# Optimization experiments

Measured on AMD Instinct MI355X. Metric: run time of the kernel, lower is better.

The kernel has to match this reference:

```python
import jax, jax.numpy as jnp
import numpy as np

IN_F = 4096
OUT_F = 4096
RANK = 16
ALPHA = 32
BLOCK = 64  # quantization blocksize along in_features
SCALING = ALPHA / RANK


def setup_inputs() -> dict:
    key = jax.random.key(0)
    k1, k2, k3, k4, k5, k6 = jax.random.split(key, 6)
    x = jax.random.normal(k1, (4, 2048, IN_F), dtype=jnp.float32)
    # int4 codes stored with +8 offset, values in [0, 16)
    q_codes = jax.random.randint(k2, (OUT_F, IN_F), 0, 16, dtype=jnp.int32)
    # per-(row, block) dequant scales
    scales = jax.random.uniform(k3, (OUT_F, IN_F // BLOCK), dtype=jnp.float32) * 0.02
    bias = jax.random.normal(k4, (OUT_F,), dtype=jnp.float32) * 0.02
    lora_A = jax.random.normal(k5, (RANK, IN_F), dtype=jnp.float32) * (1.0 / np.sqrt(IN_F))
    lora_B = jax.random.normal(k6, (OUT_F, RANK), dtype=jnp.float32) * 0.02
    return {"x": x, "q_codes": q_codes, "scales": scales, "bias": bias,
            "lora_A": lora_A, "lora_B": lora_B}


def _dequant(q_codes, scales):
    # [O, I] int4 codes (offset by 8) -> fp32 weight via blockwise scales
    O, I = q_codes.shape
    c = (q_codes.astype(jnp.float32) - 8.0).reshape(O, I // BLOCK, BLOCK)
    return (c * scales[:, :, None]).reshape(O, I)


def reference(x, q_codes, scales, bias, lora_A, lora_B):
    w = _dequant(q_codes, scales)                      # [O, I]
    base = jnp.einsum('bsi,oi->bso', x, w) + bias      # dequant GEMM + bias
    # LoRA branch: dropout(p=0) is identity; x @ (B@A).T == (x @ A.T) @ B.T
    lora = jnp.einsum('bsr,or->bso', jnp.einsum('bsi,ri->bsr', x, lora_A), lora_B)
    return base + lora * SCALING
```

## Files before the change

kernel.cpp:

```cpp
#include <hip/hip_runtime.h>
#include <hip/hip_bf16.h>

#define IN_F   4096
#define OUT_F  4096
#define RANK   16
#define M_TOK  8192
#define SCALING 2.0f

typedef __attribute__((ext_vector_type(8))) short short8;
typedef __attribute__((ext_vector_type(4))) float f32x4;
typedef __attribute__((ext_vector_type(4))) float fvec4;
typedef __attribute__((ext_vector_type(4))) int   ivec4;
typedef __attribute__((ext_vector_type(4))) unsigned int uvec4;

__global__ __launch_bounds__(256) void prep_fused(const float* __restrict__ x,
                                                  __hip_bfloat16* __restrict__ xb,
                                                  const int* __restrict__ q,
                                                  const float* __restrict__ sc,
                                                  const float* __restrict__ lA,
                                                  const float* __restrict__ lB,
                                                  __hip_bfloat16* __restrict__ W) {
    const int bid = blockIdx.x;
    if ((bid & 1) == 0) {
        size_t i = ((size_t)(bid >> 1) * 256 + threadIdx.x) * 8;
        fvec4 a = __builtin_nontemporal_load((const fvec4*)(x + i));
        fvec4 b = __builtin_nontemporal_load((const fvec4*)(x + i + 4));
        union { uvec4 u; __hip_bfloat16 h[8]; } p;
        p.h[0] = __float2bfloat16(a.x);
        p.h[1] = __float2bfloat16(a.y);
        p.h[2] = __float2bfloat16(a.z);
        p.h[3] = __float2bfloat16(a.w);
        p.h[4] = __float2bfloat16(b.x);
        p.h[5] = __float2bfloat16(b.y);
        p.h[6] = __float2bfloat16(b.z);
        p.h[7] = __float2bfloat16(b.w);
        *(uvec4*)(xb + i) = p.u;
    } else {
        const int db = bid >> 1;
        const int o  = db >> 2;
        const int i0 = (db & 3) * 1024 + threadIdx.x * 4;

        float b[RANK];
#pragma unroll
        for (int r = 0; r < RANK; ++r) b[r] = lB[o * RANK + r];

        ivec4 qv = __builtin_nontemporal_load((const ivec4*)(q + (size_t)o * IN_F + i0));
        float s  = sc[o * (IN_F / 64) + (i0 >> 6)];

        float l0 = 0.f, l1 = 0.f, l2 = 0.f, l3 = 0.f;
#pragma unroll
        for (int r = 0; r < RANK; ++r) {
            fvec4 av = *(const fvec4*)(lA + (size_t)r * IN_F + i0);
            l0 += b[r] * av.x; l1 += b[r] * av.y;
            l2 += b[r] * av.z; l3 += b[r] * av.w;
        }
        union { ushort4 u; __hip_bfloat16 h[4]; } p;
        p.h[0] = __float2bfloat16((float)(qv.x - 8) * s + SCALING * l0);
        p.h[1] = __float2bfloat16((float)(qv.y - 8) * s + SCALING * l1);
        p.h[2] = __float2bfloat16((float)(qv.z - 8) * s + SCALING * l2);
        p.h[3] = __float2bfloat16((float)(qv.w - 8) * s + SCALING * l3);
        *(ushort4*)(W + (size_t)o * IN_F + i0) = p.u;
    }
}


__device__ __forceinline__ void load_lds16(const void* g, void* l) {
    __builtin_amdgcn_global_load_lds(
        (const __attribute__((address_space(1))) unsigned int*)g,
        (__attribute__((address_space(3))) unsigned int*)l, 16, 0, 0);
}

#define MFMA_BF16 __builtin_amdgcn_mfma_f32_16x16x32_bf16

__global__ __launch_bounds__(512, 2) void gemm256_8ph(const __hip_bfloat16* __restrict__ A,
                                                      const __hip_bfloat16* __restrict__ B,
                                                      const float* __restrict__ bias,
                                                      float* __restrict__ C) {
    extern __shared__ __align__(16) char lds[];

    const int tid  = threadIdx.x;
    const int lane = tid & 63;
    const int wave = tid >> 6;

    const int wg = (blockIdx.x & 7) * 64 + (blockIdx.x >> 3);
    const int tm = wg >> 4;
    const int tn = wg & 15;

    const __hip_bfloat16* Ab = A + (size_t)tm * 256 * IN_F;
    const __hip_bfloat16* Bb = B + (size_t)tn * 256 * IN_F;

    const int    c0   = ((lane & 3) * 8) ^ ((lane >= 32) ? 16 : 0);
    const size_t off0 = (size_t)((wave >> 1) * 16 + (lane >> 2)) * IN_F
                      + (size_t)((wave & 1) * 32 + c0);

    const int flo = (lane & 15) * 64 + (((lane >> 4) * 16) ^ ((lane & 8) << 2));

    const int ah = wave >> 2;
    const int bh = (wave >> 1) & 1;
    const int bs = (wave & 1) * 4;

#define STAGE2(gp, lo) do {                                               \
        load_lds16((gp) + off0,             lds + (lo) + wave * 1024);    \
        load_lds16((gp) + off0 + 64 * IN_F, lds + (lo) + (8 + wave) * 1024); \
    } while (0)

    STAGE2(Bb,                    32768);
    STAGE2(Bb + 128 * IN_F,       49152);
    STAGE2(Ab,                    0);
    STAGE2(Ab + 128 * IN_F,       16384);
    STAGE2(Bb + 64,               65536 + 32768);
    STAGE2(Bb + 64 + 128 * IN_F,  65536 + 49152);
    asm volatile("s_waitcnt vmcnt(4)" ::: "memory");
    __builtin_amdgcn_s_barrier();

    short8 aF[4][2], bA[2][2], bB[2][2];
    f32x4 acc[8][4] = {};

    for (int t = 0; t < 64; ++t) {
        const int cb = (t & 1) << 16;
        const int nb = cb ^ 65536;
        const int t1 = ((t + 1) & 63) << 6;
        const int t2 = ((t + 2) & 63) << 6;
        const int aO = cb + ah * 16384;
        const int bO = cb + 32768 + bh * 16384;

#pragma unroll
        for (int i = 0; i < 4; ++i)
#pragma unroll
            for (int kk = 0; kk < 2; ++kk)
                aF[i][kk] = *(const short8*)(lds + aO + (i * 2 + kk) * 1024 + flo);
#pragma unroll
        for (int j = 0; j < 2; ++j)
#pragma unroll
            for (int kk = 0; kk < 2; ++kk)
                bA[j][kk] = *(const short8*)(lds + bO + ((bs + j) * 2 + kk) * 1024 + flo);
        STAGE2(Ab + t1, nb);
        __builtin_amdgcn_s_barrier();
        __builtin_amdgcn_s_setprio(1);
#pragma unroll
        for (int i = 0; i < 4; ++i)
#pragma unroll
            for (int j = 0; j < 2; ++j)
#pragma unroll
                for (int kk = 0; kk < 2; ++kk)
                    acc[i][j] = MFMA_BF16(aF[i][kk], bA[j][kk], acc[i][j], 0, 0, 0);
        __builtin_amdgcn_s_setprio(0);
        __builtin_amdgcn_s_barrier();

#pragma unroll
        for (int j = 0; j < 2; ++j)
#pragma unroll
            for (int kk = 0; kk < 2; ++kk)
                bB[j][kk] = *(const short8*)(lds + bO + ((bs + 2 + j) * 2 + kk) * 1024 + flo);
        STAGE2(Ab + 128 * IN_F + t1, nb + 16384);
        __builtin_amdgcn_s_barrier();
        __builtin_amdgcn_s_setprio(1);
#pragma unroll
        for (int i = 0; i < 4; ++i)
#pragma unroll
            for (int j = 0; j < 2; ++j)
#pragma unroll
                for (int kk = 0; kk < 2; ++kk)
                    acc[i][2 + j] = MFMA_BF16(aF[i][kk], bB[j][kk], acc[i][2 + j], 0, 0, 0);
        __builtin_amdgcn_s_setprio(0);
        __builtin_amdgcn_s_barrier();

#pragma unroll
        for (int i = 0; i < 4; ++i)
#pragma unroll
            for (int kk = 0; kk < 2; ++kk)
                aF[i][kk] = *(const short8*)(lds + aO + ((4 + i) * 2 + kk) * 1024 + flo);
        STAGE2(Bb + t2, cb + 32768);
        __builtin_amdgcn_s_barrier();
        __builtin_amdgcn_s_setprio(1);
#pragma unroll
        for (int i = 0; i < 4; ++i)
#pragma unroll
            for (int j = 0; j < 2; ++j)
#pragma unroll
                for (int kk = 0; kk < 2; ++kk)
                    acc[4 + i][2 + j] = MFMA_BF16(aF[i][kk], bB[j][kk], acc[4 + i][2 + j], 0, 0, 0);
        __builtin_amdgcn_s_setprio(0);
        __builtin_amdgcn_s_barrier();

        STAGE2(Bb + 128 * IN_F + t2, cb + 49152);
        asm volatile("s_waitcnt vmcnt(4)" ::: "memory");
        __builtin_amdgcn_s_barrier();
        __builtin_amdgcn_s_setprio(1);
#pragma unroll
        for (int i = 0; i < 4; ++i)
#pragma unroll
            for (int j = 0; j < 2; ++j)
#pragma unroll
                for (int kk = 0; kk < 2; ++kk)
                    acc[4 + i][j] = MFMA_BF16(aF[i][kk], bA[j][kk], acc[4 + i][j], 0, 0, 0);
        __builtin_amdgcn_s_setprio(0);
        __builtin_amdgcn_s_barrier();
    }
    asm volatile("s_waitcnt vmcnt(0)" ::: "memory");

    const int qd = lane >> 4;
    const int cl = lane & 15;
    const size_t m_base = (size_t)tm * 256 + (size_t)ah * 128;
    const int    n_base = tn * 256 + (wave & 3) * 64;
#pragma unroll
    for (int fn = 0; fn < 4; ++fn) {
        const int n = n_base + fn * 16 + cl;
        const float bv = bias[n];
#pragma unroll
        for (int fm = 0; fm < 8; ++fm) {
            const size_t m0 = m_base + fm * 16 + qd * 4;
#pragma unroll
            for (int r = 0; r < 4; ++r)
                __builtin_nontemporal_store(acc[fm][fn][r] + bv,
                                            &C[(m0 + r) * OUT_F + n]);
        }
    }
#undef STAGE2
}

extern "C" void kernel_launch(void* const* d_in, const int* in_sizes, int n_in,
                              void* d_out, int out_size, void* d_ws, size_t ws_size,
                              hipStream_t stream) {
    const float* x    = (const float*)d_in[0];
    const int*   qc   = (const int*)d_in[1];
    const float* sc   = (const float*)d_in[2];
    const float* bias = (const float*)d_in[3];
    const float* lA   = (const float*)d_in[4];
    const float* lB   = (const float*)d_in[5];
    float* out = (float*)d_out;

    __hip_bfloat16* xb = (__hip_bfloat16*)d_ws;
    __hip_bfloat16* wb = xb + (size_t)M_TOK * IN_F;

    static bool attr_done = false;
    if (!attr_done) {
        (void)hipFuncSetAttribute((const void*)gemm256_8ph,
                                  hipFuncAttributeMaxDynamicSharedMemorySize, 131072);
        attr_done = true;
    }

    prep_fused<<<32768, 256, 0, stream>>>(x, xb, qc, sc, lA, lB, wb);
    gemm256_8ph<<<dim3(512), dim3(512), 131072, stream>>>(xb, wb, bias, out);
}
```

Before: 524.1 us.

## Split prep kernel, reuse LoRA-A rows across outputs, remap GEMM tiles per XCD

```diff
diff --git a/kernel.cpp b/kernel.cpp
--- a/kernel.cpp
+++ b/kernel.cpp
@@ -13,16 +13,12 @@
 typedef __attribute__((ext_vector_type(4))) int   ivec4;
 typedef __attribute__((ext_vector_type(4))) unsigned int uvec4;
 
-__global__ __launch_bounds__(256) void prep_fused(const float* __restrict__ x,
-                                                  __hip_bfloat16* __restrict__ xb,
-                                                  const int* __restrict__ q,
-                                                  const float* __restrict__ sc,
-                                                  const float* __restrict__ lA,
-                                                  const float* __restrict__ lB,
-                                                  __hip_bfloat16* __restrict__ W) {
-    const int bid = blockIdx.x;
-    if ((bid & 1) == 0) {
-        size_t i = ((size_t)(bid >> 1) * 256 + threadIdx.x) * 8;
+__global__ __launch_bounds__(256) void cvt_x(const float* __restrict__ x,
+                                             __hip_bfloat16* __restrict__ xb) {
+    const size_t nvec = (size_t)M_TOK * IN_F / 8;
+    const size_t stride = (size_t)gridDim.x * 256;
+    for (size_t idx = (size_t)blockIdx.x * 256 + threadIdx.x; idx < nvec; idx += stride) {
+        const size_t i = idx * 8;
         fvec4 a = __builtin_nontemporal_load((const fvec4*)(x + i));
         fvec4 b = __builtin_nontemporal_load((const fvec4*)(x + i + 4));
         union { uvec4 u; __hip_bfloat16 h[8]; } p;
@@ -35,31 +31,42 @@
         p.h[6] = __float2bfloat16(b.z);
         p.h[7] = __float2bfloat16(b.w);
         *(uvec4*)(xb + i) = p.u;
-    } else {
-        const int db = bid >> 1;
-        const int o  = db >> 2;
-        const int i0 = (db & 3) * 1024 + threadIdx.x * 4;
-
-        float b[RANK];
-#pragma unroll
-        for (int r = 0; r < RANK; ++r) b[r] = lB[o * RANK + r];
-
-        ivec4 qv = __builtin_nontemporal_load((const ivec4*)(q + (size_t)o * IN_F + i0));
-        float s  = sc[o * (IN_F / 64) + (i0 >> 6)];
-
+    }
+}
+
+__global__ __launch_bounds__(256) void dequant_lora(const int* __restrict__ q,
+                                                    const float* __restrict__ sc,
+                                                    const float* __restrict__ lA,
+                                                    const float* __restrict__ lB,
+                                                    __hip_bfloat16* __restrict__ W) {
+    const int c0 = (blockIdx.x & 3) * 1024 + threadIdx.x * 4;
+    const int o0 = (blockIdx.x >> 2) * 16;
+
+    fvec4 a[RANK];
+#pragma unroll
+    for (int r = 0; r < RANK; ++r)
+        a[r] = *(const fvec4*)(lA + (size_t)r * IN_F + c0);
+
+    const float s_base = 0.f; (void)s_base;
+#pragma unroll 2
+    for (int oo = 0; oo < 16; ++oo) {
+        const int o = o0 + oo;
+        ivec4 qv = __builtin_nontemporal_load((const ivec4*)(q + (size_t)o * IN_F + c0));
+        const float s = sc[o * (IN_F / 64) + (c0 >> 6)];
+        const float* lbo = lB + o * RANK;
         float l0 = 0.f, l1 = 0.f, l2 = 0.f, l3 = 0.f;
 #pragma unroll
         for (int r = 0; r < RANK; ++r) {
-            fvec4 av = *(const fvec4*)(lA + (size_t)r * IN_F + i0);
-            l0 += b[r] * av.x; l1 += b[r] * av.y;
-            l2 += b[r] * av.z; l3 += b[r] * av.w;
+            const float br = lbo[r];
+            l0 += br * a[r].x; l1 += br * a[r].y;
+            l2 += br * a[r].z; l3 += br * a[r].w;
         }
         union { ushort4 u; __hip_bfloat16 h[4]; } p;
         p.h[0] = __float2bfloat16((float)(qv.x - 8) * s + SCALING * l0);
         p.h[1] = __float2bfloat16((float)(qv.y - 8) * s + SCALING * l1);
         p.h[2] = __float2bfloat16((float)(qv.z - 8) * s + SCALING * l2);
         p.h[3] = __float2bfloat16((float)(qv.w - 8) * s + SCALING * l3);
-        *(ushort4*)(W + (size_t)o * IN_F + i0) = p.u;
+        *(ushort4*)(W + (size_t)o * IN_F + c0) = p.u;
     }
 }
 
@@ -82,9 +89,10 @@
     const int lane = tid & 63;
     const int wave = tid >> 6;
 
-    const int wg = (blockIdx.x & 7) * 64 + (blockIdx.x >> 3);
-    const int tm = wg >> 4;
-    const int tn = wg & 15;
+    const int xcd = blockIdx.x & 7;
+    const int w64 = blockIdx.x >> 3;
+    const int tm  = (xcd >> 1) * 8 + (w64 >> 3);
+    const int tn  = (xcd & 1) * 8 + (w64 & 7);
 
     const __hip_bfloat16* Ab = A + (size_t)tm * 256 * IN_F;
     const __hip_bfloat16* Bb = B + (size_t)tn * 256 * IN_F;
@@ -240,6 +248,7 @@
         attr_done = true;
     }
 
-    prep_fused<<<32768, 256, 0, stream>>>(x, xb, qc, sc, lA, lB, wb);
+    cvt_x<<<2048, 256, 0, stream>>>(x, xb);
+    dequant_lora<<<1024, 256, 0, stream>>>(qc, sc, lA, lB, wb);
     gemm256_8ph<<<dim3(512), dim3(512), 131072, stream>>>(xb, wb, bias, out);
 }
```

New measurement: 487.5 us. 7.0% less time.
